# Performance work log

Measured on AMD Instinct MI355X. Metric: run time of the kernel, lower is better.

Reference implementation:

```python
import jax, jax.numpy as jnp
import numpy as np

SQRT2 = 1.4142135623730951  # lrelu def_gain
LRELU_SLOPE = 0.2
EPS = 1e-8


def setup_inputs() -> dict:
    key = jax.random.key(0)
    k1, k2, k3, k4 = jax.random.split(key, 4)
    B, C_in, C_out, H, W, K, DLAT = 8, 512, 512, 32, 32, 3, 512
    x = jax.random.normal(k1, (B, C_in, H, W), dtype=jnp.float32)
    y = jax.random.normal(k2, (B, DLAT), dtype=jnp.float32)
    # init_std = 1.0 since use_wscale=True, lrmul=1
    weight = jax.random.normal(k3, (C_out, C_in, K, K), dtype=jnp.float32)
    mod_weight = jax.random.normal(k4, (C_in, DLAT), dtype=jnp.float32)
    bias = jnp.ones((C_in,), dtype=jnp.float32)
    return {"x": x, "y": y, "weight": weight, "mod_weight": mod_weight, "bias": bias}


def reference(x, y, weight, mod_weight, bias):
    B, C_in, H, W = x.shape
    C_out, _, K, _ = weight.shape
    dlat = mod_weight.shape[1]
    w_mul_mod = dlat ** (-0.5)  # EqualizedLinear wscale; conv w_mul is unused in forward
    # style: s = sqrt(2) * lrelu(y @ W_mod^T + b)
    s = y @ (mod_weight * w_mul_mod).T  # [B, C_in]
    s = jax.nn.leaky_relu(s + bias, LRELU_SLOPE) * SQRT2
    # modulate per-sample weights: [B, C_out, C_in, K, K]
    ww = weight[None] * s[:, None, :, None, None]
    # demodulate
    d = jax.lax.rsqrt(jnp.sum(ww * ww, axis=(2, 3, 4)) + EPS)  # [B, C_out]
    ww = ww * d[:, :, None, None, None]
    # fused grouped conv: groups = batch
    xg = x.reshape(1, B * C_in, H, W)
    wg = ww.reshape(B * C_out, C_in, K, K)
    out = jax.lax.conv_general_dilated(
        xg, wg, window_strides=(1, 1), padding="SAME",
        dimension_numbers=("NCHW", "OIHW", "NCHW"),
        feature_group_count=B)
    return out.reshape(B, C_out, H, W)
```

## Files before the change

kernel.cpp:

```cpp
#include <hip/hip_runtime.h>
#include <hip/hip_bf16.h>

typedef float f32x4 __attribute__((ext_vector_type(4)));
typedef short bf16x8 __attribute__((ext_vector_type(8)));

#define LRELU_SLOPE 0.2f
#define SQRT2F 1.4142135623730951f
#define MODSCALE 0.044194173824159216f

#define GLL(SRC, DST)                                                       \
  __builtin_amdgcn_global_load_lds(                                         \
      (const __attribute__((address_space(1))) unsigned int*)(SRC),         \
      (__attribute__((address_space(3))) unsigned int*)(DST), 16, 0, 0)

__global__ __launch_bounds__(256) void prep_kernel(const float* __restrict__ w,
                                                   const float* __restrict__ y,
                                                   const float* __restrict__ mw,
                                                   const float* __restrict__ bias,
                                                   __hip_bfloat16* __restrict__ wt2,
                                                   float* __restrict__ wsq,
                                                   float* __restrict__ s,
                                                   __hip_bfloat16* __restrict__ xsp) {
  const int bid = blockIdx.x;
  const int tid = threadIdx.x;
  if (bid < 1024) {
    int idx = bid * 256 + tid;
    int co = idx >> 9, ci = idx & 511;
    const float* p = w + (size_t)idx * 9;
    float v[9];
    float sq = 0.f;
#pragma unroll
    for (int t = 0; t < 9; ++t) {
      v[t] = p[t];
      sq += v[t] * v[t];
    }
    wsq[idx] = sq;
    int slabbase = ((ci >> 6) * 2 + ((ci >> 5) & 1)) * 16384 + co * 32 + (ci & 31);
#pragma unroll
    for (int t = 0; t < 9; ++t)
      wt2[t * 262144 + slabbase] = __float2bfloat16(v[t]);
  } else if (bid < 1152) {
    int l = tid & 63;
    int ci = (bid - 1024) * 4 + (tid >> 6);
    const float4* mwr = reinterpret_cast<const float4*>(mw + ci * 512);
    float4 m0 = mwr[2 * l], m1 = mwr[2 * l + 1];
    float acc[8];
#pragma unroll
    for (int b = 0; b < 8; ++b) {
      const float4* yr = reinterpret_cast<const float4*>(y + b * 512);
      float4 y0 = yr[2 * l], y1 = yr[2 * l + 1];
      acc[b] = m0.x * y0.x + m0.y * y0.y + m0.z * y0.z + m0.w * y0.w +
               m1.x * y1.x + m1.y * y1.y + m1.z * y1.z + m1.w * y1.w;
    }
#pragma unroll
    for (int off = 32; off > 0; off >>= 1) {
#pragma unroll
      for (int b = 0; b < 8; ++b) acc[b] += __shfl_xor(acc[b], off, 64);
    }
    if (l < 8) {
      float v = acc[l] * MODSCALE + bias[ci];
      v = v > 0.f ? v : LRELU_SLOPE * v;
      s[l * 512 + ci] = v * SQRT2F;
    }
  } else {
    int i = (bid - 1152) * 256 + tid;
    int b = i / 8448;
    int r = i - b * 8448;
    int pos = r >> 6;
    int cj = (r & 63) << 3;
    int hr, hc;
    if (pos < 34) { hr = 0; hc = pos; }
    else if (pos < 68) { hr = 33; hc = pos - 34; }
    else if (pos < 100) { hr = pos - 67; hc = 0; }
    else { hr = pos - 99; hc = 33; }
    unsigned off = (unsigned)((b * 34 + hr) * 34 + hc) * 512 + cj;
    int4 z = {0, 0, 0, 0};
    *reinterpret_cast<int4*>(xsp + off) = z;
  }
}

__global__ __launch_bounds__(256) void xsdem_kernel(const float* __restrict__ x,
                                                    const float* __restrict__ s,
                                                    const float* __restrict__ wsq,
                                                    __hip_bfloat16* __restrict__ xsp,
                                                    float* __restrict__ d) {
  const int bid = blockIdx.x;
  const int tid = threadIdx.x;
  if (bid < 2048) {
    int cc = bid & 7;
    int h = (bid >> 3) & 31;
    int b = bid >> 8;
    __shared__ __hip_bfloat16 tile[32][72];
    int cil = tid >> 2;
    int w0 = (tid & 3) * 8;
    int ci = cc * 64 + cil;
    const float* xp = x + (((size_t)(b * 512 + ci) * 32 + h) << 5) + w0;
    float sv = s[b * 512 + ci];
    float4 a0 = *reinterpret_cast<const float4*>(xp);
    float4 a1 = *reinterpret_cast<const float4*>(xp + 4);
    tile[w0 + 0][cil] = __float2bfloat16(a0.x * sv);
    tile[w0 + 1][cil] = __float2bfloat16(a0.y * sv);
    tile[w0 + 2][cil] = __float2bfloat16(a0.z * sv);
    tile[w0 + 3][cil] = __float2bfloat16(a0.w * sv);
    tile[w0 + 4][cil] = __float2bfloat16(a1.x * sv);
    tile[w0 + 5][cil] = __float2bfloat16(a1.y * sv);
    tile[w0 + 6][cil] = __float2bfloat16(a1.z * sv);
    tile[w0 + 7][cil] = __float2bfloat16(a1.w * sv);
    __syncthreads();
    int wloc = tid >> 3;
    int cj = (tid & 7) * 8;
    int4 v = *reinterpret_cast<const int4*>(&tile[wloc][cj]);
    unsigned off = (unsigned)((b * 34 + h + 1) * 34 + (wloc + 1)) * 512 + cc * 64 + cj;
    *reinterpret_cast<int4*>(xsp + off) = v;
  } else {
    int l = tid & 63;
    int co = (bid - 2048) * 4 + (tid >> 6);
    const float4* qr = reinterpret_cast<const float4*>(wsq + co * 512);
    float4 q0 = qr[2 * l], q1 = qr[2 * l + 1];
    float acc[8];
#pragma unroll
    for (int b = 0; b < 8; ++b) {
      const float4* sr = reinterpret_cast<const float4*>(s + b * 512);
      float4 s0 = sr[2 * l], s1 = sr[2 * l + 1];
      acc[b] = q0.x * s0.x * s0.x + q0.y * s0.y * s0.y + q0.z * s0.z * s0.z +
               q0.w * s0.w * s0.w + q1.x * s1.x * s1.x + q1.y * s1.y * s1.y +
               q1.z * s1.z * s1.z + q1.w * s1.w * s1.w;
    }
#pragma unroll
    for (int off = 32; off > 0; off >>= 1) {
#pragma unroll
      for (int b = 0; b < 8; ++b) acc[b] += __shfl_xor(acc[b], off, 64);
    }
    if (l < 8) d[l * 512 + co] = rsqrtf(acc[l] + 1e-8f);
  }
}

__global__ __launch_bounds__(256, 2) void conv_kernel(const __hip_bfloat16* __restrict__ xsp,
                                                      const __hip_bfloat16* __restrict__ wt2,
                                                      const float* __restrict__ dmod,
                                                      float* __restrict__ out) {
  __shared__ __hip_bfloat16 As_[2][224 * 64];
  const int bid = blockIdx.x;
  const int xcd = bid & 7, slot = bid >> 3;
  const int bmq = slot >> 3;
  const int bn = slot & 7;
  const int bb = xcd;
  const int tid = threadIdx.x;
  const int wv = tid >> 6;
  const int l = tid & 63;
  const int wr = wv >> 1, wc = wv & 1;
  const int h0 = bmq << 2;

  unsigned ahoff[7];
  int adst[7];
#pragma unroll
  for (int j = 0; j < 7; ++j) {
    int rb = j * 32 + wv * 8;
    int r = rb + (l >> 3);
    int rc = r > 203 ? 203 : r;
    int hr = rc / 34, hc = rc - hr * 34;
    ahoff[j] = (unsigned)((bb * 34 + h0 + hr) * 34 + hc) * 512 + (((l & 7) ^ (r & 7)) << 3);
    adst[j] = rb;
  }
  int pb[4];
#pragma unroll
  for (int m = 0; m < 4; ++m)
    pb[m] = ((wr << 1) + (m >> 1)) * 34 + ((m & 1) << 4) + (l & 15);

  const char* wtb = reinterpret_cast<const char*>(wt2);
  const unsigned nbase = (unsigned)(bn << 12) + (wc << 11) + ((l & 15) << 6) + ((l >> 4) << 4);

  f32x4 acc[2][4];
#pragma unroll
  for (int n = 0; n < 2; ++n)
#pragma unroll
    for (int m = 0; m < 4; ++m) acc[n][m] = (f32x4)0.f;

  bf16x8 fbk[2][2][2];

  auto stageA1 = [&](__hip_bfloat16* An, int j, int kn) {
    GLL(xsp + ahoff[j] + kn * 64, An + (adst[j] << 6));
  };
  auto loadB = [&](int bank, int t, int c) {
#pragma unroll
    for (int kh = 0; kh < 2; ++kh) {
      const char* base = wtb + (size_t)(((t * 8 + c) * 2 + kh) << 15) + nbase;
#pragma unroll
      for (int n = 0; n < 2; ++n)
        fbk[bank][kh][n] = *reinterpret_cast<const bf16x8*>(base + (n << 10));
    }
  };
  auto doTap = [&](int bank, const __hip_bfloat16* Aq, int dh, int dw) {
#pragma unroll
    for (int kh = 0; kh < 2; ++kh) {
      const int cb = (kh << 2) + (l >> 4);
      bf16x8 af[4];
#pragma unroll
      for (int m = 0; m < 4; ++m) {
        int p = pb[m] + dh * 34 + dw;
        af[m] = *reinterpret_cast<const bf16x8*>(Aq + p * 64 + ((cb ^ (p & 7)) << 3));
      }
      __builtin_amdgcn_s_setprio(1);
#pragma unroll
      for (int n = 0; n < 2; ++n)
#pragma unroll
        for (int m = 0; m < 4; ++m)
          acc[n][m] = __builtin_amdgcn_mfma_f32_16x16x32_bf16(fbk[bank][kh][n], af[m],
                                                              acc[n][m], 0, 0, 0);
      __builtin_amdgcn_s_setprio(0);
    }
  };
  auto chunkBody = [&](int c, int P, bool stA, bool last) {
    const __hip_bfloat16* Aq = &As_[P][0];
    __hip_bfloat16* An = &As_[P ^ 1][0];
#pragma unroll
    for (int t = 0; t < 9; ++t) {
      if (!last || t < 8) loadB((P + t + 1) & 1, (t + 1) % 9, t < 8 ? c : c + 1);
      if (stA && t == 0) {
#pragma unroll
        for (int j = 0; j < 7; ++j) stageA1(An, j, c + 1);
        __builtin_amdgcn_sched_barrier(0);
      }
      doTap((P + t) & 1, Aq, t / 3, t % 3);
    }
    if (!last) {
      asm volatile("s_waitcnt vmcnt(4)" ::: "memory");
      __builtin_amdgcn_s_barrier();
      __builtin_amdgcn_sched_barrier(0);
    }
  };

#pragma unroll
  for (int j = 0; j < 7; ++j) stageA1(&As_[0][0], j, 0);
  __builtin_amdgcn_sched_barrier(0);
  loadB(0, 0, 0);
  asm volatile("s_waitcnt vmcnt(4)" ::: "memory");
  __builtin_amdgcn_s_barrier();
  __builtin_amdgcn_sched_barrier(0);

#pragma unroll 1
  for (int kp = 0; kp < 3; ++kp) {
    chunkBody(2 * kp, 0, true, false);
    chunkBody(2 * kp + 1, 1, true, false);
  }
  chunkBody(6, 0, true, false);
  chunkBody(7, 1, false, true);

  const int pixbase = (bmq << 7) + (wr << 6) + (l & 15);
  const int cob = (bn << 6) + (wc << 5) + ((l >> 4) << 2);
  float* ob = out + ((size_t)bb << 19);
  const float* drow = dmod + bb * 512;
#pragma unroll
  for (int n = 0; n < 2; ++n) {
#pragma unroll
    for (int jj = 0; jj < 4; ++jj) {
      const int co = cob + (n << 4) + jj;
      const float dv = drow[co];
      float* orow = ob + ((unsigned)co << 10) + pixbase;
#pragma unroll
      for (int m = 0; m < 4; ++m) orow[m << 4] = acc[n][m][jj] * dv;
    }
  }
}

extern "C" void kernel_launch(void* const* d_in, const int* in_sizes, int n_in,
                              void* d_out, int out_size, void* d_ws, size_t ws_size,
                              hipStream_t stream) {
  (void)in_sizes; (void)n_in; (void)out_size; (void)ws_size;
  const float* x = (const float*)d_in[0];
  const float* y = (const float*)d_in[1];
  const float* w = (const float*)d_in[2];
  const float* mw = (const float*)d_in[3];
  const float* bias = (const float*)d_in[4];
  float* out = (float*)d_out;

  char* ws = (char*)d_ws;
  float* s = (float*)(ws + 0);
  float* dmod = (float*)(ws + 16384);
  float* wsq = (float*)(ws + 32768);
  __hip_bfloat16* wt2 = (__hip_bfloat16*)(ws + 1081344);
  __hip_bfloat16* xsp = (__hip_bfloat16*)(ws + 5799936);

  prep_kernel<<<1416, 256, 0, stream>>>(w, y, mw, bias, wt2, wsq, s, xsp);
  xsdem_kernel<<<2176, 256, 0, stream>>>(x, s, wsq, xsp, dmod);
  conv_kernel<<<512, 256, 0, stream>>>(xsp, wt2, dmod, out);
}
```

Baseline: 59.17 us.

## Merge x-scaling into prep kernel and compute demod factors inside conv

Drops the separate xsdem launch. Prep blocks for x-scaling now recompute the style vector locally from mod_weight and y, then scale and transpose 8 rows of x each. The conv kernel computes its 64 demodulation factors at block start from wsq and s, which prep produces in the prior launch. This removes one kernel launch and its dependency barrier, at the cost of redundant style dot products across blocks and a short prologue added to every conv block.

After: 82.75 us. +39.9%, slower.

```diff
diff --git a/kernel.cpp b/kernel.cpp
--- a/kernel.cpp
+++ b/kernel.cpp
@@ -13,14 +13,15 @@
       (const __attribute__((address_space(1))) unsigned int*)(SRC),         \
       (__attribute__((address_space(3))) unsigned int*)(DST), 16, 0, 0)
 
-__global__ __launch_bounds__(256) void prep_kernel(const float* __restrict__ w,
-                                                   const float* __restrict__ y,
-                                                   const float* __restrict__ mw,
-                                                   const float* __restrict__ bias,
-                                                   __hip_bfloat16* __restrict__ wt2,
-                                                   float* __restrict__ wsq,
-                                                   float* __restrict__ s,
-                                                   __hip_bfloat16* __restrict__ xsp) {
+__global__ __launch_bounds__(256) void mega_prep_kernel(const float* __restrict__ w,
+                                                        const float* __restrict__ y,
+                                                        const float* __restrict__ mw,
+                                                        const float* __restrict__ bias,
+                                                        const float* __restrict__ x,
+                                                        __hip_bfloat16* __restrict__ wt2,
+                                                        float* __restrict__ wsq,
+                                                        float* __restrict__ s,
+                                                        __hip_bfloat16* __restrict__ xsp) {
   const int bid = blockIdx.x;
   const int tid = threadIdx.x;
   if (bid < 1024) {
@@ -62,7 +63,7 @@
       v = v > 0.f ? v : LRELU_SLOPE * v;
       s[l * 512 + ci] = v * SQRT2F;
     }
-  } else {
+  } else if (bid < 1416) {
     int i = (bid - 1152) * 256 + tid;
     int b = i / 8448;
     int r = i - b * 8448;
@@ -76,70 +77,71 @@
     unsigned off = (unsigned)((b * 34 + hr) * 34 + hc) * 512 + cj;
     int4 z = {0, 0, 0, 0};
     *reinterpret_cast<int4*>(xsp + off) = z;
-  }
-}
-
-__global__ __launch_bounds__(256) void xsdem_kernel(const float* __restrict__ x,
-                                                    const float* __restrict__ s,
-                                                    const float* __restrict__ wsq,
-                                                    __hip_bfloat16* __restrict__ xsp,
-                                                    float* __restrict__ d) {
-  const int bid = blockIdx.x;
-  const int tid = threadIdx.x;
-  if (bid < 2048) {
-    int cc = bid & 7;
-    int h = (bid >> 3) & 31;
-    int b = bid >> 8;
+  } else {
+    int bid2 = bid - 1416;
+    int b = bid2 >> 5;
+    int cc = (bid2 >> 2) & 7;
+    int hq = bid2 & 3;
     __shared__ __hip_bfloat16 tile[32][72];
-    int cil = tid >> 2;
-    int w0 = (tid & 3) * 8;
-    int ci = cc * 64 + cil;
-    const float* xp = x + (((size_t)(b * 512 + ci) * 32 + h) << 5) + w0;
-    float sv = s[b * 512 + ci];
-    float4 a0 = *reinterpret_cast<const float4*>(xp);
-    float4 a1 = *reinterpret_cast<const float4*>(xp + 4);
-    tile[w0 + 0][cil] = __float2bfloat16(a0.x * sv);
-    tile[w0 + 1][cil] = __float2bfloat16(a0.y * sv);
-    tile[w0 + 2][cil] = __float2bfloat16(a0.z * sv);
-    tile[w0 + 3][cil] = __float2bfloat16(a0.w * sv);
-    tile[w0 + 4][cil] = __float2bfloat16(a1.x * sv);
-    tile[w0 + 5][cil] = __float2bfloat16(a1.y * sv);
-    tile[w0 + 6][cil] = __float2bfloat16(a1.z * sv);
-    tile[w0 + 7][cil] = __float2bfloat16(a1.w * sv);
+    __shared__ float part[64][4];
+    __shared__ float s_lds[64];
+    const int cil = tid >> 2;
+    const int q = tid & 3;
+    const int ci = cc * 64 + cil;
+    {
+      const float4* mwr = reinterpret_cast<const float4*>(mw + ci * 512) + q * 32;
+      const float4* yr = reinterpret_cast<const float4*>(y + b * 512) + q * 32;
+      float p = 0.f;
+#pragma unroll
+      for (int k = 0; k < 32; ++k) {
+        float4 a = mwr[k], c = yr[k];
+        p += a.x * c.x + a.y * c.y + a.z * c.z + a.w * c.w;
+      }
+      part[cil][q] = p;
+    }
     __syncthreads();
-    int wloc = tid >> 3;
-    int cj = (tid & 7) * 8;
-    int4 v = *reinterpret_cast<const int4*>(&tile[wloc][cj]);
-    unsigned off = (unsigned)((b * 34 + h + 1) * 34 + (wloc + 1)) * 512 + cc * 64 + cj;
-    *reinterpret_cast<int4*>(xsp + off) = v;
-  } else {
-    int l = tid & 63;
-    int co = (bid - 2048) * 4 + (tid >> 6);
-    const float4* qr = reinterpret_cast<const float4*>(wsq + co * 512);
-    float4 q0 = qr[2 * l], q1 = qr[2 * l + 1];
-    float acc[8];
-#pragma unroll
-    for (int b = 0; b < 8; ++b) {
-      const float4* sr = reinterpret_cast<const float4*>(s + b * 512);
-      float4 s0 = sr[2 * l], s1 = sr[2 * l + 1];
-      acc[b] = q0.x * s0.x * s0.x + q0.y * s0.y * s0.y + q0.z * s0.z * s0.z +
-               q0.w * s0.w * s0.w + q1.x * s1.x * s1.x + q1.y * s1.y * s1.y +
-               q1.z * s1.z * s1.z + q1.w * s1.w * s1.w;
-    }
-#pragma unroll
-    for (int off = 32; off > 0; off >>= 1) {
-#pragma unroll
-      for (int b = 0; b < 8; ++b) acc[b] += __shfl_xor(acc[b], off, 64);
-    }
-    if (l < 8) d[l * 512 + co] = rsqrtf(acc[l] + 1e-8f);
+    if (tid < 64) {
+      float v = (part[tid][0] + part[tid][1] + part[tid][2] + part[tid][3]) * MODSCALE +
+                bias[cc * 64 + tid];
+      v = v > 0.f ? v : LRELU_SLOPE * v;
+      s_lds[tid] = v * SQRT2F;
+    }
+    __syncthreads();
+    const float sv = s_lds[cil];
+    const int w0 = q * 8;
+#pragma unroll 1
+    for (int hh = 0; hh < 8; ++hh) {
+      const int h = hq * 8 + hh;
+      const float* xp = x + (((size_t)(b * 512 + ci) * 32 + h) << 5) + w0;
+      float4 a0 = *reinterpret_cast<const float4*>(xp);
+      float4 a1 = *reinterpret_cast<const float4*>(xp + 4);
+      tile[w0 + 0][cil] = __float2bfloat16(a0.x * sv);
+      tile[w0 + 1][cil] = __float2bfloat16(a0.y * sv);
+      tile[w0 + 2][cil] = __float2bfloat16(a0.z * sv);
+      tile[w0 + 3][cil] = __float2bfloat16(a0.w * sv);
+      tile[w0 + 4][cil] = __float2bfloat16(a1.x * sv);
+      tile[w0 + 5][cil] = __float2bfloat16(a1.y * sv);
+      tile[w0 + 6][cil] = __float2bfloat16(a1.z * sv);
+      tile[w0 + 7][cil] = __float2bfloat16(a1.w * sv);
+      __syncthreads();
+      int wloc = tid >> 3;
+      int cj = (tid & 7) * 8;
+      int4 v = *reinterpret_cast<const int4*>(&tile[wloc][cj]);
+      unsigned off = (unsigned)((b * 34 + h + 1) * 34 + (wloc + 1)) * 512 + cc * 64 + cj;
+      *reinterpret_cast<int4*>(xsp + off) = v;
+      __syncthreads();
+    }
   }
 }
 
 __global__ __launch_bounds__(256, 2) void conv_kernel(const __hip_bfloat16* __restrict__ xsp,
                                                       const __hip_bfloat16* __restrict__ wt2,
-                                                      const float* __restrict__ dmod,
+                                                      const float* __restrict__ wsq,
+                                                      const float* __restrict__ s,
                                                       float* __restrict__ out) {
   __shared__ __hip_bfloat16 As_[2][224 * 64];
+  __shared__ float dpart[64][4];
+  __shared__ float dmodl[64];
   const int bid = blockIdx.x;
   const int xcd = bid & 7, slot = bid >> 3;
   const int bmq = slot >> 3;
@@ -151,6 +153,23 @@
   const int wr = wv >> 1, wc = wv & 1;
   const int h0 = bmq << 2;
 
+  {
+    const int co_l = tid >> 2, q = tid & 3;
+    const float4* qr = reinterpret_cast<const float4*>(wsq + ((bn << 6) + co_l) * 512) + q * 32;
+    const float4* sr = reinterpret_cast<const float4*>(s + bb * 512) + q * 32;
+    float p = 0.f;
+#pragma unroll
+    for (int k = 0; k < 32; ++k) {
+      float4 a = qr[k], c = sr[k];
+      p += a.x * c.x * c.x + a.y * c.y * c.y + a.z * c.z * c.z + a.w * c.w * c.w;
+    }
+    dpart[co_l][q] = p;
+  }
+  __syncthreads();
+  if (tid < 64)
+    dmodl[tid] = rsqrtf(dpart[tid][0] + dpart[tid][1] + dpart[tid][2] + dpart[tid][3] + 1e-8f);
+  __syncthreads();
+
   unsigned ahoff[7];
   int adst[7];
 #pragma unroll
@@ -247,16 +266,15 @@
   chunkBody(7, 1, false, true);
 
   const int pixbase = (bmq << 7) + (wr << 6) + (l & 15);
-  const int cob = (bn << 6) + (wc << 5) + ((l >> 4) << 2);
+  const int cobl = (wc << 5) + ((l >> 4) << 2);
   float* ob = out + ((size_t)bb << 19);
-  const float* drow = dmod + bb * 512;
 #pragma unroll
   for (int n = 0; n < 2; ++n) {
 #pragma unroll
     for (int jj = 0; jj < 4; ++jj) {
-      const int co = cob + (n << 4) + jj;
-      const float dv = drow[co];
-      float* orow = ob + ((unsigned)co << 10) + pixbase;
+      const int col = cobl + (n << 4) + jj;
+      const float dv = dmodl[col];
+      float* orow = ob + ((unsigned)((bn << 6) + col) << 10) + pixbase;
 #pragma unroll
       for (int m = 0; m < 4; ++m) orow[m << 4] = acc[n][m][jj] * dv;
     }
@@ -276,12 +294,10 @@
 
   char* ws = (char*)d_ws;
   float* s = (float*)(ws + 0);
-  float* dmod = (float*)(ws + 16384);
   float* wsq = (float*)(ws + 32768);
   __hip_bfloat16* wt2 = (__hip_bfloat16*)(ws + 1081344);
   __hip_bfloat16* xsp = (__hip_bfloat16*)(ws + 5799936);
 
-  prep_kernel<<<1416, 256, 0, stream>>>(w, y, mw, bias, wt2, wsq, s, xsp);
-  xsdem_kernel<<<2176, 256, 0, stream>>>(x, s, wsq, xsp, dmod);
-  conv_kernel<<<512, 256, 0, stream>>>(xsp, wt2, dmod, out);
+  mega_prep_kernel<<<1672, 256, 0, stream>>>(w, y, mw, bias, x, wt2, wsq, s, xsp);
+  conv_kernel<<<512, 256, 0, stream>>>(xsp, wt2, wsq, s, out);
 }
```
